# Kernel tuning notes

Hardware: AMD Instinct MI355X
Metric: run time of the kernel (lower is better)

The kernel has to match this reference:

```python
import jax, jax.numpy as jnp
import numpy as np

N = 100000
IN_DIM = 128
OUT_DIM = 128
E = 320000


def setup_inputs() -> dict:
    key = jax.random.key(0)
    ks = jax.random.split(key, 12)
    x = jax.random.normal(ks[0], (N, IN_DIM), dtype=jnp.float32)
    src0 = jax.random.randint(ks[1], (E,), 0, N)
    dst0 = jax.random.randint(ks[2], (E,), 0, N)
    src1 = jax.random.randint(ks[3], (E,), 0, N)
    dst1 = jax.random.randint(ks[4], (E,), 0, N)
    s = 1.0 / np.sqrt(IN_DIM)
    W0 = jax.random.uniform(ks[5], (IN_DIM, OUT_DIM), minval=-s, maxval=s)
    b0 = jax.random.uniform(ks[6], (OUT_DIM,), minval=-s, maxval=s)
    W1 = jax.random.uniform(ks[7], (IN_DIM, OUT_DIM), minval=-s, maxval=s)
    b1 = jax.random.uniform(ks[8], (OUT_DIM,), minval=-s, maxval=s)
    sa = 1.0 / np.sqrt(2 * OUT_DIM)
    a0 = jax.random.uniform(ks[9], (2 * OUT_DIM,), minval=-sa, maxval=sa)
    a1 = jax.random.uniform(ks[10], (2 * OUT_DIM,), minval=-sa, maxval=sa)
    return {"x": x, "src0": src0, "dst0": dst0, "src1": src1, "dst1": dst1,
            "W0": W0, "b0": b0, "a0": a0, "W1": W1, "b1": b1, "a1": a1}


def _rel_gat(x, src, dst, W, b, a):
    # wh = Linear(in_dim, out_dim)(x)  -> [N, D]
    wh = x @ W + b
    D = wh.shape[1]
    # e = leaky_relu(a^T [wh_src || wh_dst]) ; split a instead of concat on edges
    e = jax.nn.leaky_relu(wh[src] @ a[:D] + wh[dst] @ a[D:])  # [E]
    # segment softmax over incoming edges of each dst node
    m = jax.ops.segment_max(e, dst, num_segments=N)
    ex = jnp.exp(e - m[dst])
    denom = jax.ops.segment_sum(ex, dst, num_segments=N)
    alpha = ex / denom[dst]  # [E]
    # weighted scatter-sum of src features (zero for isolated dst nodes)
    return jax.ops.segment_sum(alpha[:, None] * wh[src], dst, num_segments=N)


def reference(x, src0, dst0, src1, dst1, W0, b0, a0, W1, b1, a1):
    h0 = _rel_gat(x, src0, dst0, W0, b0, a0)
    h1 = _rel_gat(x, src1, dst1, W1, b1, a1)
    # cross-relation 'sum' reducer
    return h0 + h1
```

## Files before the change

### kernel.cpp

```cpp
#include <hip/hip_runtime.h>
#include <hip/hip_bf16.h>


typedef __bf16 bf16x8 __attribute__((ext_vector_type(8)));
typedef float f32x4 __attribute__((ext_vector_type(4)));

#define DIM 128
#define NP 4
#define NR 32
#define RANK_BLOCKS (NP * NR)
#define HIST_BINS 6400

__global__ __launch_bounds__(256) void prep_w_kernel(
    const float* __restrict__ W0, const float* __restrict__ W1,
    __bf16* __restrict__ wtf)
{
    const int e = blockIdx.x * 256 + threadIdx.x;
    if (e >= 4096) return;
    const int lane = e & 63;
    const int ko4  = (e >> 6) & 3;
    const int ct   = (e >> 8) & 7;
    const int rel  = e >> 11;
    const float* W = rel ? W1 : W0;
    const int n  = ct * 16 + (lane & 15);
    const int k0 = ko4 * 32 + (lane >> 4) * 8;
    bf16x8 v;
#pragma unroll
    for (int j = 0; j < 8; ++j) v[j] = (__bf16)W[(k0 + j) * DIM + n];
    *(bf16x8*)(wtf + (size_t)e * 8) = v;
}

__global__ __launch_bounds__(256) void rank_hist_kernel(
    const int* __restrict__ dst0, const int* __restrict__ dst1,
    unsigned* __restrict__ partial, unsigned* __restrict__ rank,
    int N, int E)
{
    __shared__ unsigned hist_[HIST_BINS];
    const int tid = threadIdx.x;
    const int p    = blockIdx.x & (NP - 1);
    const int r    = blockIdx.x >> 2;
    const int rel  = r >> 4;
    const int rr   = r & 15;
    const int rngsz = (N + 15) / 16;
    const int lo = rr * rngsz;
    const int hi = min(lo + rngsz, N);
    const int nbins = hi - lo;
    for (int j = tid; j < nbins; j += 256) hist_[j] = 0u;
    __syncthreads();

    const int chunk = (E + NP - 1) / NP;
    const int e0 = p * chunk;
    const int e1 = min(e0 + chunk, E);
    const int* dsts = rel ? dst1 : dst0;
    unsigned* rk = rank + (rel ? E : 0);

    for (int i = e0 + tid * 4; i < e1; i += 1024) {
        if (i + 3 < e1) {
            const int4 v = *(const int4*)(dsts + i);
            if (v.x >= lo && v.x < hi) rk[i]     = atomicAdd(&hist_[v.x - lo], 1u);
            if (v.y >= lo && v.y < hi) rk[i + 1] = atomicAdd(&hist_[v.y - lo], 1u);
            if (v.z >= lo && v.z < hi) rk[i + 2] = atomicAdd(&hist_[v.z - lo], 1u);
            if (v.w >= lo && v.w < hi) rk[i + 3] = atomicAdd(&hist_[v.w - lo], 1u);
        } else {
            for (int j = i; j < e1; ++j) {
                const int d = dsts[j];
                if (d >= lo && d < hi) rk[j] = atomicAdd(&hist_[d - lo], 1u);
            }
        }
    }
    __syncthreads();
    unsigned* part = partial + (size_t)p * (2 * N) + (size_t)rel * N + lo;
    for (int j = tid; j < nbins; j += 256) part[j] = hist_[j];
}

__global__ __launch_bounds__(256) void gemm_wh_kernel(
    const float* __restrict__ x, const __bf16* __restrict__ wtf,
    const float* __restrict__ b0, const float* __restrict__ b1,
    const float* __restrict__ a0, const float* __restrict__ a1,
    __bf16* __restrict__ wh, float* __restrict__ s_src,
    float* __restrict__ s_dst, int N)
{
    __shared__ __align__(16) __bf16 Cst[64 * 136];
    const int tid = threadIdx.x;

    const int lane = tid & 63;
    const int wave = tid >> 6;
    const int quad = lane >> 4;
    const int mr   = lane & 15;

    const long row0 = (long)blockIdx.x * 64 + wave * 16;
    long arow = row0 + mr;
    if (arow >= N) arow = N - 1;
    const f32x4* xr = (const f32x4*)(x + arow * DIM);

    bf16x8 afrag[4];
#pragma unroll
    for (int ko4 = 0; ko4 < 4; ++ko4) {
        f32x4 lo = xr[ko4 * 8 + quad * 2], hi = xr[ko4 * 8 + quad * 2 + 1];
        afrag[ko4] = (bf16x8){ (__bf16)lo.x, (__bf16)lo.y, (__bf16)lo.z, (__bf16)lo.w,
                               (__bf16)hi.x, (__bf16)hi.y, (__bf16)hi.z, (__bf16)hi.w };
    }

    const bf16x8* wt = (const bf16x8*)wtf;

#pragma unroll
    for (int rel = 0; rel < 2; ++rel) {
        f32x4 zero = {0.f, 0.f, 0.f, 0.f};
        f32x4 acc[8];
#pragma unroll
        for (int t = 0; t < 8; ++t) acc[t] = zero;

#pragma unroll
        for (int ko4 = 0; ko4 < 4; ++ko4) {
#pragma unroll
            for (int ct = 0; ct < 8; ++ct) {
                bf16x8 bfrag = wt[((rel * 8 + ct) * 4 + ko4) * 64 + lane];
                acc[ct] = __builtin_amdgcn_mfma_f32_16x16x32_bf16(afrag[ko4], bfrag, acc[ct], 0, 0, 0);
            }
        }

        const float* bias = rel ? b1 : b0;
        const float* a    = rel ? a1 : a0;
        float psr[4] = {0.f, 0.f, 0.f, 0.f};
        float pdr[4] = {0.f, 0.f, 0.f, 0.f};
#pragma unroll
        for (int ct = 0; ct < 8; ++ct) {
            const int c = ct * 16 + mr;
            const float bn = bias[c];
            const float asc = a[c], adc = a[DIM + c];
#pragma unroll
            for (int rr = 0; rr < 4; ++rr) {
                const float wv = acc[ct][rr] + bn;
                Cst[(wave * 16 + quad * 4 + rr) * 136 + c] = (__bf16)wv;
                psr[rr] += asc * wv;
                pdr[rr] += adc * wv;
            }
        }
#pragma unroll
        for (int off = 1; off < 16; off <<= 1) {
#pragma unroll
            for (int rr = 0; rr < 4; ++rr) {
                psr[rr] += __shfl_xor(psr[rr], off);
                pdr[rr] += __shfl_xor(pdr[rr], off);
            }
        }
        if (mr == 0) {
#pragma unroll
            for (int rr = 0; rr < 4; ++rr) {
                const long orow = row0 + quad * 4 + rr;
                if (orow < N) {
                    s_src[(size_t)rel * N + orow] = psr[rr];
                    s_dst[(size_t)rel * N + orow] = pdr[rr];
                }
            }
        }
        __syncthreads();
#pragma unroll
        for (int i = 0; i < 4; ++i) {
            const int chunk = tid + 256 * i;
            const int row = chunk >> 4, c8 = chunk & 15;
            bf16x8 v = *(const bf16x8*)&Cst[row * 136 + c8 * 8];
            const long grow = (long)blockIdx.x * 64 + row;
            if (grow < N)
                *(bf16x8*)(wh + ((size_t)rel * N + grow) * DIM + c8 * 8) = v;
        }
        __syncthreads();
    }
}

__global__ __launch_bounds__(256) void scanA_kernel(
    const unsigned* __restrict__ partial, unsigned* __restrict__ tmp,
    unsigned* __restrict__ bsum, int n)
{
    __shared__ unsigned s[256];
    const int t = threadIdx.x;
    const int i = blockIdx.x * 256 + t;
    unsigned v = 0u;
    if (i < n) {
#pragma unroll
        for (int p = 0; p < NP; ++p) v += partial[(size_t)p * n + i];
    }
    s[t] = v;
    __syncthreads();
#pragma unroll
    for (int off = 1; off < 256; off <<= 1) {
        unsigned add = (t >= off) ? s[t - off] : 0u;
        __syncthreads();
        s[t] += add;
        __syncthreads();
    }
    if (i < n) tmp[i] = s[t] - v;
    if (t == 255) bsum[blockIdx.x] = s[t];
}

__global__ __launch_bounds__(256) void scan2_kernel(
    const unsigned* __restrict__ tmp, const unsigned* __restrict__ bsum,
    const unsigned* __restrict__ partial, unsigned* __restrict__ rowptr,
    int n, int nb)
{
    __shared__ unsigned s[256];
    __shared__ unsigned ex[1024];
    const int t = threadIdx.x;
    unsigned loc[4], sum = 0u;
#pragma unroll
    for (int k = 0; k < 4; ++k) {
        int idx = t * 4 + k;
        loc[k] = (idx < nb) ? bsum[idx] : 0u;
        sum += loc[k];
    }
    s[t] = sum;
    __syncthreads();
#pragma unroll
    for (int off = 1; off < 256; off <<= 1) {
        unsigned add = (t >= off) ? s[t - off] : 0u;
        __syncthreads();
        s[t] += add;
        __syncthreads();
    }
    unsigned run = s[t] - sum;
#pragma unroll
    for (int k = 0; k < 4; ++k) {
        ex[t * 4 + k] = run;
        run += loc[k];
    }
    __syncthreads();
    const unsigned pref = ex[blockIdx.x];
    const int i = blockIdx.x * 256 + t;
    if (i < n) {
        unsigned val = tmp[i] + pref;
        rowptr[i] = val;
        if (i == n - 1) {
            unsigned dsum = 0u;
#pragma unroll
            for (int p = 0; p < NP; ++p) dsum += partial[(size_t)p * n + i];
            rowptr[n] = val + dsum;
        }
    }
}

__global__ __launch_bounds__(256) void fill_kernel(
    const int* __restrict__ src0, const int* __restrict__ dst0,
    const int* __restrict__ src1, const int* __restrict__ dst1,
    const float* __restrict__ s_src, const float* __restrict__ s_dst,
    const unsigned* __restrict__ rowptr, const unsigned* __restrict__ rank,
    const unsigned* __restrict__ partial,
    uint2* __restrict__ sorted, int N, int E)
{
    const int i = blockIdx.x * 256 + threadIdx.x;
    if (i >= E) return;
    const int s0 = src0[i], d0 = dst0[i];
    const int s1 = src1[i], d1 = dst1[i];

    const int chunk = (E + NP - 1) / NP;
    const int p = i / chunk;
    const int n2 = 2 * N;
    unsigned off0 = 0u, off1 = 0u;
    for (int q = 0; q < p; ++q) {
        off0 += partial[(size_t)q * n2 + d0];
        off1 += partial[(size_t)q * n2 + N + d1];
    }
    const unsigned p0 = rowptr[d0] + off0 + rank[i];
    const unsigned p1 = rowptr[N + d1] + off1 + rank[E + i];

    float v0 = s_src[s0] + s_dst[d0];
    v0 = v0 > 0.f ? v0 : 0.01f * v0;
    const float e0 = __expf(v0);
    float v1 = s_src[N + s1] + s_dst[N + d1];
    v1 = v1 > 0.f ? v1 : 0.01f * v1;
    const float e1 = __expf(v1);

    sorted[p0] = make_uint2((unsigned)s0, __float_as_uint(e0));
    sorted[p1] = make_uint2((unsigned)s1, __float_as_uint(e1));
}

__global__ __launch_bounds__(256) void aggregate_kernel(
    const unsigned* __restrict__ rowptr, const uint2* __restrict__ sorted,
    const __bf16* __restrict__ wh, float* __restrict__ out, int N)
{
    const int tid  = threadIdx.x;
    const int lane = tid & 63;
    const int sub  = lane >> 4;
    const int mr   = lane & 15;
    int d = blockIdx.x * 4 + (tid >> 6);
    if (d >= N) return;
    d = __builtin_amdgcn_readfirstlane(d);

    const unsigned beg0 = rowptr[d],     end0 = rowptr[d + 1];
    const unsigned beg1 = rowptr[N + d], end1 = rowptr[N + d + 1];
    const unsigned len0 = end0 - beg0;
    const unsigned T    = len0 + (end1 - beg1);

    float acc0[8], acc1[8], l0 = 0.f, l1 = 0.f;
#pragma unroll
    for (int k = 0; k < 8; ++k) { acc0[k] = 0.f; acc1[k] = 0.f; }

    const size_t whstride = (size_t)N * DIM;

    for (unsigned t0 = 0; t0 < T; t0 += 8) {
        const unsigned tA = t0 + sub, tB = tA + 4;
        const bool vA = tA < T, vB = tB < T;
        const bool rA = tA >= len0, rB = tB >= len0;

        unsigned iA = rA ? beg1 + (tA - len0) : beg0 + tA;
        unsigned iB = rB ? beg1 + (tB - len0) : beg0 + tB;
        iA = vA ? iA : 0u;
        iB = vB ? iB : 0u;

        const uint2 eA = sorted[iA];
        const uint2 eB = sorted[iB];

        const float evA = vA ? __uint_as_float(eA.y) : 0.f;
        const float evB = vB ? __uint_as_float(eB.y) : 0.f;
        const float wA0 = rA ? 0.f : evA, wA1 = rA ? evA : 0.f;
        const float wB0 = rB ? 0.f : evB, wB1 = rB ? evB : 0.f;
        l0 += wA0 + wB0;
        l1 += wA1 + wB1;

        const bf16x8 wA = *(const bf16x8*)(wh + (rA ? whstride : 0)
                                              + (size_t)eA.x * DIM + mr * 8);
        const bf16x8 wB = *(const bf16x8*)(wh + (rB ? whstride : 0)
                                              + (size_t)eB.x * DIM + mr * 8);
#pragma unroll
        for (int k = 0; k < 8; ++k) {
            const float fA = (float)wA[k], fB = (float)wB[k];
            acc0[k] += wA0 * fA + wB0 * fB;
            acc1[k] += wA1 * fA + wB1 * fB;
        }
    }

#pragma unroll
    for (int k = 0; k < 8; ++k) {
        acc0[k] += __shfl_xor(acc0[k], 16);
        acc0[k] += __shfl_xor(acc0[k], 32);
        acc1[k] += __shfl_xor(acc1[k], 16);
        acc1[k] += __shfl_xor(acc1[k], 32);
    }
    l0 += __shfl_xor(l0, 16); l0 += __shfl_xor(l0, 32);
    l1 += __shfl_xor(l1, 16); l1 += __shfl_xor(l1, 32);

    const float inv0 = l0 > 0.f ? 1.f / l0 : 0.f;
    const float inv1 = l1 > 0.f ? 1.f / l1 : 0.f;

    if (sub == 0) {
        float o[8];
#pragma unroll
        for (int k = 0; k < 8; ++k) o[k] = acc0[k] * inv0 + acc1[k] * inv1;
        float4 v0 = {o[0], o[1], o[2], o[3]};
        float4 v1 = {o[4], o[5], o[6], o[7]};
        float* op = out + (size_t)d * DIM + mr * 8;
        *(float4*)op       = v0;
        *(float4*)(op + 4) = v1;
    }
}

extern "C" void kernel_launch(void* const* d_in, const int* in_sizes, int n_in,
                              void* d_out, int out_size, void* d_ws, size_t ws_size,
                              hipStream_t stream) {
    const float* x = (const float*)d_in[0];
    const int* srcs[2] = {(const int*)d_in[1], (const int*)d_in[3]};
    const int* dsts[2] = {(const int*)d_in[2], (const int*)d_in[4]};
    const float* Ws[2] = {(const float*)d_in[5], (const float*)d_in[8]};
    const float* Bs[2] = {(const float*)d_in[6], (const float*)d_in[9]};
    const float* As[2] = {(const float*)d_in[7], (const float*)d_in[10]};

    const int N = in_sizes[0] / DIM;
    const int E = in_sizes[1];
    const int n2 = 2 * N;
    const int nb = (n2 + 255) / 256;
    float* out = (float*)d_out;

    char* p = (char*)d_ws;
    __bf16*   wh      = (__bf16*)p;   p += (size_t)n2 * DIM * 2;
    __bf16*   wtf     = (__bf16*)p;   p += (size_t)4096 * 8 * 2;
    float*    s_src   = (float*)p;    p += (size_t)n2 * 4;
    float*    s_dst   = (float*)p;    p += (size_t)n2 * 4;
    unsigned* partial = (unsigned*)p; p += (size_t)NP * n2 * 4;
    unsigned* tmp     = (unsigned*)p; p += (size_t)n2 * 4;
    unsigned* rowptr  = (unsigned*)p; p += (size_t)(n2 + 2) * 4;
    unsigned* rank    = (unsigned*)p; p += (size_t)2 * E * 4;
    uint2*    sorted  = (uint2*)p;    p += (size_t)2 * E * 8;
    unsigned* bsum    = (unsigned*)p; p += (size_t)nb * 4;

    prep_w_kernel<<<16, 256, 0, stream>>>(Ws[0], Ws[1], wtf);
    rank_hist_kernel<<<RANK_BLOCKS, 256, 0, stream>>>(
        dsts[0], dsts[1], partial, rank, N, E);
    gemm_wh_kernel<<<(N + 63) / 64, 256, 0, stream>>>(
        x, wtf, Bs[0], Bs[1], As[0], As[1], wh, s_src, s_dst, N);
    scanA_kernel<<<nb, 256, 0, stream>>>(partial, tmp, bsum, n2);
    scan2_kernel<<<nb, 256, 0, stream>>>(tmp, bsum, partial, rowptr, n2, nb);
    fill_kernel<<<(E + 255) / 256, 256, 0, stream>>>(
        srcs[0], dsts[0], srcs[1], dsts[1], s_src, s_dst,
        rowptr, rank, partial, sorted, N, E);
    aggregate_kernel<<<(N + 3) / 4, 256, 0, stream>>>(
        rowptr, sorted, wh, out, N);
}
```

Baseline: 253.0 us.

## Widen rank histogram grid and precompute per-partition offsets in scan

Result: faster. 231.3 us (-8.6%).

```diff
diff --git a/kernel.cpp b/kernel.cpp
--- a/kernel.cpp
+++ b/kernel.cpp
@@ -6,10 +6,10 @@
 typedef float f32x4 __attribute__((ext_vector_type(4)));
 
 #define DIM 128
-#define NP 4
-#define NR 32
-#define RANK_BLOCKS (NP * NR)
-#define HIST_BINS 6400
+#define NP 8
+#define NR 64
+#define RANK_BLOCKS (NP * NR * 2)
+#define HIST_BINS 1568
 
 __global__ __launch_bounds__(256) void prep_w_kernel(
     const float* __restrict__ W0, const float* __restrict__ W1,
@@ -38,13 +38,14 @@
     __shared__ unsigned hist_[HIST_BINS];
     const int tid = threadIdx.x;
     const int p    = blockIdx.x & (NP - 1);
-    const int r    = blockIdx.x >> 2;
-    const int rel  = r >> 4;
-    const int rr   = r & 15;
-    const int rngsz = (N + 15) / 16;
+    const int r    = blockIdx.x >> 3;
+    const int rel  = r >> 6;
+    const int rr   = r & (NR - 1);
+    const int rngsz = (N + NR - 1) / NR;
     const int lo = rr * rngsz;
     const int hi = min(lo + rngsz, N);
     const int nbins = hi - lo;
+    if (nbins <= 0) return;
     for (int j = tid; j < nbins; j += 256) hist_[j] = 0u;
     __syncthreads();
 
@@ -169,7 +170,7 @@
 }
 
 __global__ __launch_bounds__(256) void scanA_kernel(
-    const unsigned* __restrict__ partial, unsigned* __restrict__ tmp,
+    unsigned* __restrict__ partial, unsigned* __restrict__ tmp,
     unsigned* __restrict__ bsum, int n)
 {
     __shared__ unsigned s[256];
@@ -177,8 +178,14 @@
     const int i = blockIdx.x * 256 + t;
     unsigned v = 0u;
     if (i < n) {
-#pragma unroll
-        for (int p = 0; p < NP; ++p) v += partial[(size_t)p * n + i];
+        unsigned run = 0u;
+#pragma unroll
+        for (int p = 0; p < NP; ++p) {
+            const unsigned c = partial[(size_t)p * n + i];
+            partial[(size_t)p * n + i] = run;
+            run += c;
+        }
+        v = run;
     }
     s[t] = v;
     __syncthreads();
@@ -195,8 +202,7 @@
 
 __global__ __launch_bounds__(256) void scan2_kernel(
     const unsigned* __restrict__ tmp, const unsigned* __restrict__ bsum,
-    const unsigned* __restrict__ partial, unsigned* __restrict__ rowptr,
-    int n, int nb)
+    unsigned* __restrict__ rowptr, int n, int nb, unsigned total)
 {
     __shared__ unsigned s[256];
     __shared__ unsigned ex[1024];
@@ -227,14 +233,8 @@
     const unsigned pref = ex[blockIdx.x];
     const int i = blockIdx.x * 256 + t;
     if (i < n) {
-        unsigned val = tmp[i] + pref;
-        rowptr[i] = val;
-        if (i == n - 1) {
-            unsigned dsum = 0u;
-#pragma unroll
-            for (int p = 0; p < NP; ++p) dsum += partial[(size_t)p * n + i];
-            rowptr[n] = val + dsum;
-        }
+        rowptr[i] = tmp[i] + pref;
+        if (i == n - 1) rowptr[n] = total;
     }
 }
 
@@ -254,11 +254,8 @@
     const int chunk = (E + NP - 1) / NP;
     const int p = i / chunk;
     const int n2 = 2 * N;
-    unsigned off0 = 0u, off1 = 0u;
-    for (int q = 0; q < p; ++q) {
-        off0 += partial[(size_t)q * n2 + d0];
-        off1 += partial[(size_t)q * n2 + N + d1];
-    }
+    const unsigned off0 = partial[(size_t)p * n2 + d0];
+    const unsigned off1 = partial[(size_t)p * n2 + N + d1];
     const unsigned p0 = rowptr[d0] + off0 + rank[i];
     const unsigned p1 = rowptr[N + d1] + off1 + rank[E + i];
 
@@ -387,7 +384,8 @@
     gemm_wh_kernel<<<(N + 63) / 64, 256, 0, stream>>>(
         x, wtf, Bs[0], Bs[1], As[0], As[1], wh, s_src, s_dst, N);
     scanA_kernel<<<nb, 256, 0, stream>>>(partial, tmp, bsum, n2);
-    scan2_kernel<<<nb, 256, 0, stream>>>(tmp, bsum, partial, rowptr, n2, nb);
+    scan2_kernel<<<nb, 256, 0, stream>>>(tmp, bsum, rowptr, n2, nb,
+                                         (unsigned)(2 * E));
     fill_kernel<<<(E + 255) / 256, 256, 0, stream>>>(
         srcs[0], dsts[0], srcs[1], dsts[1], s_src, s_dst,
         rowptr, rank, partial, sorted, N, E);
```
